# Kernel tuning notes

Hardware: AMD Instinct MI355X
Metric: run time of the kernel (lower is better)

Reference implementation:

```python
import jax, jax.numpy as jnp
import numpy as np

N_EMBD = 512
HEAD_SIZE = 64
B, T = 256, 256


def setup_inputs() -> dict:
    key = jax.random.key(0)
    ks = jax.random.split(key, 7)
    s = 1.0 / np.sqrt(N_EMBD)
    return {
        "x": jax.random.normal(ks[0], (B, T, N_EMBD), dtype=jnp.float32),
        "Wk": jax.random.uniform(ks[1], (N_EMBD, HEAD_SIZE), jnp.float32, -s, s),
        "bk": jax.random.uniform(ks[2], (HEAD_SIZE,), jnp.float32, -s, s),
        "Wq": jax.random.uniform(ks[3], (N_EMBD, HEAD_SIZE), jnp.float32, -s, s),
        "bq": jax.random.uniform(ks[4], (HEAD_SIZE,), jnp.float32, -s, s),
        "Wv": jax.random.uniform(ks[5], (N_EMBD, HEAD_SIZE), jnp.float32, -s, s),
        "bv": jax.random.uniform(ks[6], (HEAD_SIZE,), jnp.float32, -s, s),
    }


def reference(x, Wk, bk, Wq, bq, Wv, bv):
    # Single-head causal self-attention (dropout = identity in eval mode).
    Bq, Tq, C = x.shape
    k = x @ Wk + bk        # [B, T, H]
    q = x @ Wq + bq        # [B, T, H]
    v = x @ Wv + bv        # [B, T, H]
    scale = 1.0 / jnp.sqrt(jnp.asarray(k.shape[-1], x.dtype))
    scores = jnp.einsum('bth,bsh->bts', q, k) * scale  # [B, T, T]
    causal = jnp.tril(jnp.ones((Tq, Tq), dtype=bool))
    scores = jnp.where(causal, scores, -jnp.inf)
    attn = jax.nn.softmax(scores, axis=-1)
    return jnp.einsum('bts,bsh->bth', attn, v)  # [B, T, H]
```

## Files before the change

### kernel.cpp

```cpp
#include <hip/hip_runtime.h>
#include <stdint.h>

typedef __attribute__((ext_vector_type(8))) short bf16x8;
typedef __attribute__((ext_vector_type(4))) float f32x4;

#if __has_builtin(__builtin_amdgcn_exp2f)
#define EXP2F(x) __builtin_amdgcn_exp2f(x)
#else
#define EXP2F(x) exp2f(x)
#endif

__device__ __forceinline__ short f2bf(float f) {
    union { float f; uint32_t u; } c; c.f = f;
    return (short)((c.u + 0x7fffu + ((c.u >> 16) & 1u)) >> 16);
}

__global__ void prep_kernel(const float* __restrict__ Wk, const float* __restrict__ bk,
                            const float* __restrict__ Wq, const float* __restrict__ bq,
                            const float* __restrict__ Wv, const float* __restrict__ bv,
                            short* __restrict__ Wt, float* __restrict__ bcat) {
    const int col = blockIdx.x;
    const float* W; const float* bb; int c0;
    if (col < 64)       { W = Wk; bb = bk; c0 = col; }
    else if (col < 128) { W = Wq; bb = bq; c0 = col - 64; }
    else                { W = Wv; bb = bv; c0 = col - 128; }
    for (int c = threadIdx.x; c < 512; c += blockDim.x)
        Wt[col * 512 + c] = f2bf(W[(size_t)c * 64 + c0]);
    if (threadIdx.x == 0) bcat[col] = bb[c0];
}

__global__ __launch_bounds__(256, 2) void qkv_kernel(
    const float* __restrict__ x, const short* __restrict__ Wt,
    const float* __restrict__ bcat,
    short* __restrict__ Kb, short* __restrict__ Qb, short* __restrict__ Vb) {
    const int tid = threadIdx.x;
    const int wave = tid >> 6, lane = tid & 63;
    const int quad = lane >> 4, l16 = lane & 15;
    const int row0 = blockIdx.x * 128 + wave * 32;

    f32x4 acc[2][12];
#pragma unroll
    for (int m = 0; m < 2; m++)
#pragma unroll
        for (int i = 0; i < 12; i++) acc[m][i] = (f32x4){0.f, 0.f, 0.f, 0.f};

    const float* xr0 = x + (size_t)(row0 + l16) * 512 + quad * 8;
    const float* xr1 = xr0 + (size_t)16 * 512;

    float4 p00 = ((const float4*)xr0)[0];
    float4 p01 = ((const float4*)xr0)[1];
    float4 p10 = ((const float4*)xr1)[0];
    float4 p11 = ((const float4*)xr1)[1];

    for (int c = 0; c < 16; c++) {
        bf16x8 a0, a1;
        a0[0]=f2bf(p00.x); a0[1]=f2bf(p00.y); a0[2]=f2bf(p00.z); a0[3]=f2bf(p00.w);
        a0[4]=f2bf(p01.x); a0[5]=f2bf(p01.y); a0[6]=f2bf(p01.z); a0[7]=f2bf(p01.w);
        a1[0]=f2bf(p10.x); a1[1]=f2bf(p10.y); a1[2]=f2bf(p10.z); a1[3]=f2bf(p10.w);
        a1[4]=f2bf(p11.x); a1[5]=f2bf(p11.y); a1[6]=f2bf(p11.z); a1[7]=f2bf(p11.w);
        if (c < 15) {
            const float* n0 = xr0 + (c + 1) * 32;
            const float* n1 = xr1 + (c + 1) * 32;
            p00 = ((const float4*)n0)[0];
            p01 = ((const float4*)n0)[1];
            p10 = ((const float4*)n1)[0];
            p11 = ((const float4*)n1)[1];
        }
#pragma unroll
        for (int nt = 0; nt < 12; nt++) {
            bf16x8 bfrag = *(const bf16x8*)&Wt[(nt*16 + l16)*512 + c*32 + quad*8];
            acc[0][nt] = __builtin_amdgcn_mfma_f32_16x16x32_bf16(a0, bfrag, acc[0][nt], 0, 0, 0);
            acc[1][nt] = __builtin_amdgcn_mfma_f32_16x16x32_bf16(a1, bfrag, acc[1][nt], 0, 0, 0);
        }
    }

#pragma unroll
    for (int m = 0; m < 2; m++) {
        const int rowbase = row0 + m*16 + quad*4;
#pragma unroll
        for (int nt = 0; nt < 12; nt++) {
            const int col = nt*16 + l16;
            const float bias = bcat[col];
            short* dst = (nt < 4) ? Kb : (nt < 8) ? Qb : Vb;
            const int h = col & 63;
#pragma unroll
            for (int r = 0; r < 4; r++)
                dst[(size_t)(rowbase + r)*64 + h] = f2bf(acc[m][nt][r] + bias);
        }
    }
}

#define KSTR 72
#define VSTR 72
#define PSTR 40

__global__ __launch_bounds__(256, 2) void attn_kernel(
    const short* __restrict__ Kb, const short* __restrict__ Qb,
    const short* __restrict__ Vb, float* __restrict__ out) {
    __shared__ __align__(16) short Ks[256 * KSTR];
    __shared__ __align__(16) short Vt[2][64 * VSTR];
    __shared__ __align__(16) short Ps[4][16 * PSTR];

    const int j = blockIdx.x;
    const int b = blockIdx.y;
    const int tid = threadIdx.x;
    const int wave = tid >> 6, lane = tid & 63;
    const int quad = lane >> 4, l16 = lane & 15;
    const int ntiles = 4 * (j + 1);
    const int nchunks = j + 1;
    const size_t bbase = (size_t)b * (256 * 64);

    const int qrow = j*64 + wave*16 + l16;
    const bf16x8 qf0 = *(const bf16x8*)&Qb[bbase + (size_t)qrow*64 + quad*8];
    const bf16x8 qf1 = *(const bf16x8*)&Qb[bbase + (size_t)qrow*64 + 32 + quad*8];

    {
        const int r = tid >> 2, seg = tid & 3;
        for (int rb = 0; rb < nchunks; rb++) {
            const int row = rb*64 + r;
            const uint4* src = (const uint4*)&Kb[bbase + (size_t)row*64 + seg*16];
            uint4 a0 = src[0], a1 = src[1];
            *(uint4*)&Ks[row*KSTR + seg*16]     = a0;
            *(uint4*)&Ks[row*KSTR + seg*16 + 8] = a1;
        }
    }
    const int vs0 = (tid >> 3) * 2;
    const int vh  = tid & 7;
    uint32_t vregs[8];
    const uint16_t* Vbu = (const uint16_t*)Vb;
#pragma unroll
    for (int i = 0; i < 8; i++) {
        uint32_t lo = Vbu[bbase + (size_t)vs0*64 + vh + 8*i];
        uint32_t hi = Vbu[bbase + (size_t)(vs0 + 1)*64 + vh + 8*i];
        vregs[i] = lo | (hi << 16);
    }
#pragma unroll
    for (int i = 0; i < 8; i++)
        *(uint32_t*)&Vt[0][(vh + 8*i)*VSTR + vs0] = vregs[i];
    __syncthreads();

    f32x4 St[16];
#pragma unroll
    for (int i = 0; i < 16; i++) St[i] = (f32x4){0.f, 0.f, 0.f, 0.f};
#pragma unroll
    for (int nt = 0; nt < 16; nt++) if (nt < ntiles) {
        bf16x8 kf0 = *(const bf16x8*)&Ks[(nt*16 + l16)*KSTR + quad*8];
        bf16x8 kf1 = *(const bf16x8*)&Ks[(nt*16 + l16)*KSTR + 32 + quad*8];
        St[nt] = __builtin_amdgcn_mfma_f32_16x16x32_bf16(qf0, kf0, St[nt], 0, 0, 0);
        St[nt] = __builtin_amdgcn_mfma_f32_16x16x32_bf16(qf1, kf1, St[nt], 0, 0, 0);
    }

    const float sc2 = 0.125f * 1.44269504088896340736f;
    const int rowg0 = j*64 + wave*16 + quad*4;
    float mx[4], ls[4];
#pragma unroll
    for (int r = 0; r < 4; r++) mx[r] = -3.0e38f;
#pragma unroll
    for (int nt = 0; nt < 16; nt++) if (nt < ntiles) {
        const int cs = nt*16 + l16;
#pragma unroll
        for (int r = 0; r < 4; r++) {
            float s = (cs <= rowg0 + r) ? St[nt][r] * sc2 : -3.0e38f;
            St[nt][r] = s;
            mx[r] = fmaxf(mx[r], s);
        }
    }
#pragma unroll
    for (int d = 1; d < 16; d <<= 1)
#pragma unroll
        for (int r = 0; r < 4; r++)
            mx[r] = fmaxf(mx[r], __shfl_xor(mx[r], d, 64));
#pragma unroll
    for (int r = 0; r < 4; r++) ls[r] = 0.f;
#pragma unroll
    for (int nt = 0; nt < 16; nt++) if (nt < ntiles) {
#pragma unroll
        for (int r = 0; r < 4; r++) {
            float p = EXP2F(St[nt][r] - mx[r]);
            St[nt][r] = p;
            ls[r] += p;
        }
    }
#pragma unroll
    for (int d = 1; d < 16; d <<= 1)
#pragma unroll
        for (int r = 0; r < 4; r++)
            ls[r] += __shfl_xor(ls[r], d, 64);

    f32x4 O[4];
#pragma unroll
    for (int i = 0; i < 4; i++) O[i] = (f32x4){0.f, 0.f, 0.f, 0.f};
    short* myP = Ps[wave];

#pragma unroll
    for (int c = 0; c < 4; c++) if (c < nchunks) {
        const int buf = c & 1;
        if (c + 1 < nchunks) {
#pragma unroll
            for (int i = 0; i < 8; i++) {
                uint32_t lo = Vbu[bbase + (size_t)((c+1)*64 + vs0)*64 + vh + 8*i];
                uint32_t hi = Vbu[bbase + (size_t)((c+1)*64 + vs0 + 1)*64 + vh + 8*i];
                vregs[i] = lo | (hi << 16);
            }
        }
#pragma unroll
        for (int sub = 0; sub < 2; sub++) {
#pragma unroll
            for (int t2 = 0; t2 < 2; t2++) {
                const int nt = c*4 + sub*2 + t2;
#pragma unroll
                for (int r = 0; r < 4; r++)
                    myP[(quad*4 + r)*PSTR + t2*16 + l16] = f2bf(St[nt][r]);
            }
            bf16x8 pf = *(const bf16x8*)&myP[l16*PSTR + quad*8];
#pragma unroll
            for (int ht = 0; ht < 4; ht++) {
                bf16x8 vf = *(const bf16x8*)&Vt[buf][(ht*16 + l16)*VSTR + sub*32 + quad*8];
                O[ht] = __builtin_amdgcn_mfma_f32_16x16x32_bf16(pf, vf, O[ht], 0, 0, 0);
            }
        }
        if (c + 1 < nchunks) {
#pragma unroll
            for (int i = 0; i < 8; i++)
                *(uint32_t*)&Vt[(c+1) & 1][(vh + 8*i)*VSTR + vs0] = vregs[i];
        }
        __syncthreads();
    }

    float rls[4];
#pragma unroll
    for (int r = 0; r < 4; r++) rls[r] = 1.0f / ls[r];
    const int orow0 = j*64 + wave*16 + quad*4;
#pragma unroll
    for (int ht = 0; ht < 4; ht++)
#pragma unroll
        for (int r = 0; r < 4; r++)
            out[((size_t)b*256 + orow0 + r)*64 + ht*16 + l16] = O[ht][r] * rls[r];
}

extern "C" void kernel_launch(void* const* d_in, const int* in_sizes, int n_in,
                              void* d_out, int out_size, void* d_ws, size_t ws_size,
                              hipStream_t stream) {
    const float* x  = (const float*)d_in[0];
    const float* Wk = (const float*)d_in[1];
    const float* bk = (const float*)d_in[2];
    const float* Wq = (const float*)d_in[3];
    const float* bq = (const float*)d_in[4];
    const float* Wv = (const float*)d_in[5];
    const float* bv = (const float*)d_in[6];
    float* out = (float*)d_out;

    char* ws = (char*)d_ws;
    short* Wt   = (short*)(ws);
    float* bcat = (float*)(ws + 196608);
    short* Kb   = (short*)(ws + 262144);
    short* Qb   = (short*)(ws + 262144 + 8388608);
    short* Vb   = (short*)(ws + 262144 + 16777216);

    prep_kernel<<<192, 256, 0, stream>>>(Wk, bk, Wq, bq, Wv, bv, Wt, bcat);
    qkv_kernel<<<512, 256, 0, stream>>>(x, Wt, bcat, Kb, Qb, Vb);
    attn_kernel<<<dim3(4, 256), 256, 0, stream>>>(Kb, Qb, Vb, out);
}
```

Baseline: 268.2 us.

## Stage QKV and attention operands via async global-to-LDS copies with swizzled layouts

The QKV projection now double-buffers x and weight tiles into shared memory with async global_load_lds copies and XOR swizzles, after the prep kernel rewrites the weights chunk-major. Outputs are staged in LDS so K and Q are written with wide coalesced stores, and V is written pre-transposed. The attention kernel loads K and the transposed V with async LDS copies into swizzled unpadded buffers, and launches the heaviest causal blocks first. This targets global load latency, uncoalesced 2-byte V gathers and bank conflicts, at the cost of more LDS per block (which may lower occupancy) and extra barriers.

```diff
diff --git a/kernel.cpp b/kernel.cpp
--- a/kernel.cpp
+++ b/kernel.cpp
@@ -15,28 +15,40 @@
     return (short)((c.u + 0x7fffu + ((c.u >> 16) & 1u)) >> 16);
 }
 
+typedef __attribute__((address_space(1))) void gvoid;
+typedef __attribute__((address_space(3))) void lvoid;
+__device__ __forceinline__ void async_cp16(const void* g, void* l) {
+    __builtin_amdgcn_global_load_lds((gvoid*)g, (lvoid*)l, 16, 0, 0);
+}
+
 __global__ void prep_kernel(const float* __restrict__ Wk, const float* __restrict__ bk,
                             const float* __restrict__ Wq, const float* __restrict__ bq,
                             const float* __restrict__ Wv, const float* __restrict__ bv,
-                            short* __restrict__ Wt, float* __restrict__ bcat) {
+                            short* __restrict__ Wt2g, float* __restrict__ bcat) {
     const int col = blockIdx.x;
     const float* W; const float* bb; int c0;
     if (col < 64)       { W = Wk; bb = bk; c0 = col; }
     else if (col < 128) { W = Wq; bb = bq; c0 = col - 64; }
     else                { W = Wv; bb = bv; c0 = col - 128; }
     for (int c = threadIdx.x; c < 512; c += blockDim.x)
-        Wt[col * 512 + c] = f2bf(W[(size_t)c * 64 + c0]);
+        Wt2g[(c >> 5) * (192 * 32) + col * 32 + (c & 31)] = f2bf(W[(size_t)c * 64 + c0]);
     if (threadIdx.x == 0) bcat[col] = bb[c0];
 }
 
 __global__ __launch_bounds__(256, 2) void qkv_kernel(
-    const float* __restrict__ x, const short* __restrict__ Wt,
+    const float* __restrict__ x, const short* __restrict__ Wt2g,
     const float* __restrict__ bcat,
-    short* __restrict__ Kb, short* __restrict__ Qb, short* __restrict__ Vb) {
+    short* __restrict__ Kb, short* __restrict__ Qb, short* __restrict__ Vt) {
+    __shared__ __align__(16) char smem[57344];
+#define XS(bufp)  ((float*)(smem + (bufp) * 16384))
+#define WSB(bufp) ((short*)(smem + 32768 + (bufp) * 12288))
+    short* ce = (short*)smem;
+    const int CEP = 216;
+
     const int tid = threadIdx.x;
     const int wave = tid >> 6, lane = tid & 63;
     const int quad = lane >> 4, l16 = lane & 15;
-    const int row0 = blockIdx.x * 128 + wave * 32;
+    const int row0 = blockIdx.x * 128;
 
     f32x4 acc[2][12];
 #pragma unroll
@@ -44,64 +56,114 @@
 #pragma unroll
         for (int i = 0; i < 12; i++) acc[m][i] = (f32x4){0.f, 0.f, 0.f, 0.f};
 
-    const float* xr0 = x + (size_t)(row0 + l16) * 512 + quad * 8;
-    const float* xr1 = xr0 + (size_t)16 * 512;
-
-    float4 p00 = ((const float4*)xr0)[0];
-    float4 p01 = ((const float4*)xr0)[1];
-    float4 p10 = ((const float4*)xr1)[0];
-    float4 p11 = ((const float4*)xr1)[1];
-
+    const int xr = (lane >> 3);
+    const int xsl = lane & 7;
+    const int wc = lane >> 2;
+    const int wsl = lane & 3;
+
+#define STAGE_X(cc, bufp)                                                          \
+    for (int q = 0; q < 4; q++) {                                                  \
+        const int i = wave * 4 + q;                                                \
+        const int r = i * 8 + xr;                                                  \
+        const int s = xsl ^ ((r & 3) << 1);                                        \
+        async_cp16(x + (size_t)(row0 + r) * 512 + (cc) * 32 + s * 4,               \
+                   smem + (bufp) * 16384 + i * 1024);                              \
+    }
+#define STAGE_W(cc, bufp)                                                          \
+    for (int q = 0; q < 3; q++) {                                                  \
+        const int i = wave * 3 + q;                                                \
+        const int col = i * 16 + wc;                                               \
+        const int s = wsl ^ (col & 3);                                             \
+        async_cp16(Wt2g + ((size_t)(cc) * 192 + col) * 32 + s * 8,                 \
+                   smem + 32768 + (bufp) * 12288 + i * 1024);                      \
+    }
+
+    STAGE_X(0, 0)
+    STAGE_W(0, 0)
+    __syncthreads();
+
+    const int axoff = (quad ^ (l16 & 3)) * 8;
     for (int c = 0; c < 16; c++) {
+        const int buf = c & 1;
+        if (c < 15) { STAGE_X(c + 1, buf ^ 1) STAGE_W(c + 1, buf ^ 1) }
+        const float* pa0 = XS(buf) + (wave * 32 + l16) * 32 + axoff;
+        const float* pa1 = XS(buf) + (wave * 32 + 16 + l16) * 32 + axoff;
+        f32x4 u0 = *(const f32x4*)pa0, u1 = *(const f32x4*)(pa0 + 4);
+        f32x4 u2 = *(const f32x4*)pa1, u3 = *(const f32x4*)(pa1 + 4);
         bf16x8 a0, a1;
-        a0[0]=f2bf(p00.x); a0[1]=f2bf(p00.y); a0[2]=f2bf(p00.z); a0[3]=f2bf(p00.w);
-        a0[4]=f2bf(p01.x); a0[5]=f2bf(p01.y); a0[6]=f2bf(p01.z); a0[7]=f2bf(p01.w);
-        a1[0]=f2bf(p10.x); a1[1]=f2bf(p10.y); a1[2]=f2bf(p10.z); a1[3]=f2bf(p10.w);
-        a1[4]=f2bf(p11.x); a1[5]=f2bf(p11.y); a1[6]=f2bf(p11.z); a1[7]=f2bf(p11.w);
-        if (c < 15) {
-            const float* n0 = xr0 + (c + 1) * 32;
-            const float* n1 = xr1 + (c + 1) * 32;
-            p00 = ((const float4*)n0)[0];
-            p01 = ((const float4*)n0)[1];
-            p10 = ((const float4*)n1)[0];
-            p11 = ((const float4*)n1)[1];
-        }
+#pragma unroll
+        for (int i = 0; i < 4; i++) { a0[i] = f2bf(u0[i]); a0[4+i] = f2bf(u1[i]); }
+#pragma unroll
+        for (int i = 0; i < 4; i++) { a1[i] = f2bf(u2[i]); a1[4+i] = f2bf(u3[i]); }
+        const short* wb = WSB(buf);
 #pragma unroll
         for (int nt = 0; nt < 12; nt++) {
-            bf16x8 bfrag = *(const bf16x8*)&Wt[(nt*16 + l16)*512 + c*32 + quad*8];
+            bf16x8 bfrag = *(const bf16x8*)&wb[(nt * 16 + l16) * 32 + axoff];
             acc[0][nt] = __builtin_amdgcn_mfma_f32_16x16x32_bf16(a0, bfrag, acc[0][nt], 0, 0, 0);
             acc[1][nt] = __builtin_amdgcn_mfma_f32_16x16x32_bf16(a1, bfrag, acc[1][nt], 0, 0, 0);
         }
+        __syncthreads();
     }
 
 #pragma unroll
     for (int m = 0; m < 2; m++) {
-        const int rowbase = row0 + m*16 + quad*4;
+        const int lrow = wave * 32 + m * 16 + quad * 4;
 #pragma unroll
         for (int nt = 0; nt < 12; nt++) {
-            const int col = nt*16 + l16;
+            const int col = nt * 16 + l16;
             const float bias = bcat[col];
-            short* dst = (nt < 4) ? Kb : (nt < 8) ? Qb : Vb;
-            const int h = col & 63;
 #pragma unroll
             for (int r = 0; r < 4; r++)
-                dst[(size_t)(rowbase + r)*64 + h] = f2bf(acc[m][nt][r] + bias);
-        }
-    }
-}
-
-#define KSTR 72
-#define VSTR 72
+                ce[(lrow + r) * CEP + col] = f2bf(acc[m][nt][r] + bias);
+        }
+    }
+    __syncthreads();
+
+    {
+        const int row = tid >> 1, half = tid & 1;
+        const size_t gro = (size_t)(row0 + row) * 64 + half * 32;
+#pragma unroll
+        for (int j4 = 0; j4 < 4; j4++) {
+            uint4 kv = *(const uint4*)&ce[row * CEP + half * 32 + j4 * 8];
+            *(uint4*)&Kb[gro + j4 * 8] = kv;
+            uint4 qv = *(const uint4*)&ce[row * CEP + 64 + half * 32 + j4 * 8];
+            *(uint4*)&Qb[gro + j4 * 8] = qv;
+        }
+    }
+    {
+        const int h = tid >> 2, sq = tid & 3;
+        const size_t vbase = (size_t)(row0 >> 8) * 16384 + (size_t)h * 256 + (row0 & 255) + sq * 32;
+        const uint16_t* ceu = (const uint16_t*)ce;
+#pragma unroll
+        for (int g = 0; g < 4; g++) {
+            uint4 v;
+            uint32_t* vw = (uint32_t*)&v;
+#pragma unroll
+            for (int p = 0; p < 4; p++) {
+                const int sl = sq * 32 + g * 8 + p * 2;
+                uint32_t lo = ceu[sl * CEP + 128 + h];
+                uint32_t hi = ceu[(sl + 1) * CEP + 128 + h];
+                vw[p] = lo | (hi << 16);
+            }
+            *(uint4*)&Vt[vbase + g * 8] = v;
+        }
+    }
+#undef XS
+#undef WSB
+#undef STAGE_X
+#undef STAGE_W
+}
+
 #define PSTR 40
 
 __global__ __launch_bounds__(256, 2) void attn_kernel(
     const short* __restrict__ Kb, const short* __restrict__ Qb,
-    const short* __restrict__ Vb, float* __restrict__ out) {
-    __shared__ __align__(16) short Ks[256 * KSTR];
-    __shared__ __align__(16) short Vt[2][64 * VSTR];
+    const short* __restrict__ Vt, float* __restrict__ out) {
+    __shared__ __align__(16) short Ks[256 * 64];
+    __shared__ __align__(16) short Vts[2][64 * 64];
     __shared__ __align__(16) short Ps[4][16 * PSTR];
 
-    const int j = blockIdx.x;
+    const int j = 3 - blockIdx.x;
     const int b = blockIdx.y;
     const int tid = threadIdx.x;
     const int wave = tid >> 6, lane = tid & 63;
@@ -110,33 +172,27 @@
     const int nchunks = j + 1;
     const size_t bbase = (size_t)b * (256 * 64);
 
-    const int qrow = j*64 + wave*16 + l16;
-    const bf16x8 qf0 = *(const bf16x8*)&Qb[bbase + (size_t)qrow*64 + quad*8];
-    const bf16x8 qf1 = *(const bf16x8*)&Qb[bbase + (size_t)qrow*64 + 32 + quad*8];
-
-    {
-        const int r = tid >> 2, seg = tid & 3;
-        for (int rb = 0; rb < nchunks; rb++) {
-            const int row = rb*64 + r;
-            const uint4* src = (const uint4*)&Kb[bbase + (size_t)row*64 + seg*16];
-            uint4 a0 = src[0], a1 = src[1];
-            *(uint4*)&Ks[row*KSTR + seg*16]     = a0;
-            *(uint4*)&Ks[row*KSTR + seg*16 + 8] = a1;
-        }
-    }
-    const int vs0 = (tid >> 3) * 2;
-    const int vh  = tid & 7;
-    uint32_t vregs[8];
-    const uint16_t* Vbu = (const uint16_t*)Vb;
-#pragma unroll
-    for (int i = 0; i < 8; i++) {
-        uint32_t lo = Vbu[bbase + (size_t)vs0*64 + vh + 8*i];
-        uint32_t hi = Vbu[bbase + (size_t)(vs0 + 1)*64 + vh + 8*i];
-        vregs[i] = lo | (hi << 16);
-    }
-#pragma unroll
-    for (int i = 0; i < 8; i++)
-        *(uint32_t*)&Vt[0][(vh + 8*i)*VSTR + vs0] = vregs[i];
+    const int sr = lane >> 3;
+    const int ssl = lane & 7;
+    const int ssrc = (ssl ^ sr) * 8;
+
+    for (int q = 0; q < 2 * nchunks; q++) {
+        const int i = q * 4 + wave;
+        const int row = i * 8 + sr;
+        async_cp16(Kb + bbase + (size_t)row * 64 + ssrc, (char*)Ks + i * 1024);
+    }
+#define STAGE_V(cc, bufp)                                                          \
+    for (int q = 0; q < 2; q++) {                                                  \
+        const int i = q * 4 + wave;                                                \
+        const int h = i * 8 + sr;                                                  \
+        async_cp16(Vt + (size_t)b * 16384 + (size_t)h * 256 + (cc) * 64 + ssrc,    \
+                   (char*)Vts[bufp] + i * 1024);                                   \
+    }
+    STAGE_V(0, 0)
+
+    const int qrow = j * 64 + wave * 16 + l16;
+    const bf16x8 qf0 = *(const bf16x8*)&Qb[bbase + (size_t)qrow * 64 + quad * 8];
+    const bf16x8 qf1 = *(const bf16x8*)&Qb[bbase + (size_t)qrow * 64 + 32 + quad * 8];
     __syncthreads();
 
     f32x4 St[16];
@@ -144,20 +200,21 @@
     for (int i = 0; i < 16; i++) St[i] = (f32x4){0.f, 0.f, 0.f, 0.f};
 #pragma unroll
     for (int nt = 0; nt < 16; nt++) if (nt < ntiles) {
-        bf16x8 kf0 = *(const bf16x8*)&Ks[(nt*16 + l16)*KSTR + quad*8];
-        bf16x8 kf1 = *(const bf16x8*)&Ks[(nt*16 + l16)*KSTR + 32 + quad*8];
+        const short* kr = &Ks[(nt * 16 + l16) * 64];
+        bf16x8 kf0 = *(const bf16x8*)&kr[(quad ^ (l16 & 7)) * 8];
+        bf16x8 kf1 = *(const bf16x8*)&kr[((quad + 4) ^ (l16 & 7)) * 8];
         St[nt] = __builtin_amdgcn_mfma_f32_16x16x32_bf16(qf0, kf0, St[nt], 0, 0, 0);
         St[nt] = __builtin_amdgcn_mfma_f32_16x16x32_bf16(qf1, kf1, St[nt], 0, 0, 0);
     }
 
     const float sc2 = 0.125f * 1.44269504088896340736f;
-    const int rowg0 = j*64 + wave*16 + quad*4;
+    const int rowg0 = j * 64 + wave * 16 + quad * 4;
     float mx[4], ls[4];
 #pragma unroll
     for (int r = 0; r < 4; r++) mx[r] = -3.0e38f;
 #pragma unroll
     for (int nt = 0; nt < 16; nt++) if (nt < ntiles) {
-        const int cs = nt*16 + l16;
+        const int cs = nt * 16 + l16;
 #pragma unroll
         for (int r = 0; r < 4; r++) {
             float s = (cs <= rowg0 + r) ? St[nt][r] * sc2 : -3.0e38f;
@@ -195,47 +252,36 @@
 #pragma unroll
     for (int c = 0; c < 4; c++) if (c < nchunks) {
         const int buf = c & 1;
-        if (c + 1 < nchunks) {
-#pragma unroll
-            for (int i = 0; i < 8; i++) {
-                uint32_t lo = Vbu[bbase + (size_t)((c+1)*64 + vs0)*64 + vh + 8*i];
-                uint32_t hi = Vbu[bbase + (size_t)((c+1)*64 + vs0 + 1)*64 + vh + 8*i];
-                vregs[i] = lo | (hi << 16);
+        if (c + 1 < nchunks) { STAGE_V(c + 1, buf ^ 1) }
+#pragma unroll
+        for (int sub = 0; sub < 2; sub++) {
+#pragma unroll
+            for (int t2 = 0; t2 < 2; t2++) {
+                const int nt = c * 4 + sub * 2 + t2;
+#pragma unroll
+                for (int r = 0; r < 4; r++)
+                    myP[(quad * 4 + r) * PSTR + t2 * 16 + l16] = f2bf(St[nt][r]);
             }
-        }
-#pragma unroll
-        for (int sub = 0; sub < 2; sub++) {
-#pragma unroll
-            for (int t2 = 0; t2 < 2; t2++) {
-                const int nt = c*4 + sub*2 + t2;
-#pragma unroll
-                for (int r = 0; r < 4; r++)
-                    myP[(quad*4 + r)*PSTR + t2*16 + l16] = f2bf(St[nt][r]);
-            }
-            bf16x8 pf = *(const bf16x8*)&myP[l16*PSTR + quad*8];
+            bf16x8 pf = *(const bf16x8*)&myP[l16 * PSTR + quad * 8];
 #pragma unroll
             for (int ht = 0; ht < 4; ht++) {
-                bf16x8 vf = *(const bf16x8*)&Vt[buf][(ht*16 + l16)*VSTR + sub*32 + quad*8];
+                bf16x8 vf = *(const bf16x8*)&Vts[buf][(ht * 16 + l16) * 64 +
+                                                      (((sub * 4 + quad) ^ (l16 & 7)) * 8)];
                 O[ht] = __builtin_amdgcn_mfma_f32_16x16x32_bf16(pf, vf, O[ht], 0, 0, 0);
             }
         }
-        if (c + 1 < nchunks) {
-#pragma unroll
-            for (int i = 0; i < 8; i++)
-                *(uint32_t*)&Vt[(c+1) & 1][(vh + 8*i)*VSTR + vs0] = vregs[i];
-        }
         __syncthreads();
     }
 
     float rls[4];
 #pragma unroll
     for (int r = 0; r < 4; r++) rls[r] = 1.0f / ls[r];
-    const int orow0 = j*64 + wave*16 + quad*4;
+    const int orow0 = j * 64 + wave * 16 + quad * 4;
 #pragma unroll
     for (int ht = 0; ht < 4; ht++)
 #pragma unroll
         for (int r = 0; r < 4; r++)
-            out[((size_t)b*256 + orow0 + r)*64 + ht*16 + l16] = O[ht][r] * rls[r];
+            out[((size_t)b * 256 + orow0 + r) * 64 + ht * 16 + l16] = O[ht][r] * rls[r];
 }
 
 extern "C" void kernel_launch(void* const* d_in, const int* in_sizes, int n_in,
@@ -251,13 +297,13 @@
     float* out = (float*)d_out;
 
     char* ws = (char*)d_ws;
-    short* Wt   = (short*)(ws);
+    short* Wt2g = (short*)(ws);
     float* bcat = (float*)(ws + 196608);
     short* Kb   = (short*)(ws + 262144);
     short* Qb   = (short*)(ws + 262144 + 8388608);
-    short* Vb   = (short*)(ws + 262144 + 16777216);
-
-    prep_kernel<<<192, 256, 0, stream>>>(Wk, bk, Wq, bq, Wv, bv, Wt, bcat);
-    qkv_kernel<<<512, 256, 0, stream>>>(x, Wt, bcat, Kb, Qb, Vb);
-    attn_kernel<<<dim3(4, 256), 256, 0, stream>>>(Kb, Qb, Vb, out);
-}
+    short* Vt   = (short*)(ws + 262144 + 16777216);
+
+    prep_kernel<<<192, 256, 0, stream>>>(Wk, bk, Wq, bq, Wv, bv, Wt2g, bcat);
+    qkv_kernel<<<512, 256, 0, stream>>>(x, Wt2g, bcat, Kb, Qb, Vt);
+    attn_kernel<<<dim3(4, 256), 256, 0, stream>>>(Kb, Qb, Vt, out);
+}
```

Measured after the change: 233.2 us. -13.0%, faster.

## Fuse QKV projection and causal attention into one kernel per batch

Applied to the files above, without the earlier changes.

Merges the QKV projection and attention kernels into a single kernel with one 512-thread block per batch element. K, Q and transposed V are kept in XOR-swizzled shared memory, so the bf16 K/Q/V round trip through global memory is gone. Each wave takes a pair of query tiles (t and 15-t) to even out the causal work, and the weight layout is regrouped by k-chunk for more contiguous loads. In exchange, only 256 blocks of about 106 KB shared memory each are launched, which lowers parallelism and occupancy.

```diff
diff --git a/kernel.cpp b/kernel.cpp
--- a/kernel.cpp
+++ b/kernel.cpp
@@ -18,25 +18,33 @@
 __global__ void prep_kernel(const float* __restrict__ Wk, const float* __restrict__ bk,
                             const float* __restrict__ Wq, const float* __restrict__ bq,
                             const float* __restrict__ Wv, const float* __restrict__ bv,
-                            short* __restrict__ Wt, float* __restrict__ bcat) {
+                            short* __restrict__ Wt2g, float* __restrict__ bcat) {
     const int col = blockIdx.x;
     const float* W; const float* bb; int c0;
     if (col < 64)       { W = Wk; bb = bk; c0 = col; }
     else if (col < 128) { W = Wq; bb = bq; c0 = col - 64; }
     else                { W = Wv; bb = bv; c0 = col - 128; }
     for (int c = threadIdx.x; c < 512; c += blockDim.x)
-        Wt[col * 512 + c] = f2bf(W[(size_t)c * 64 + c0]);
+        Wt2g[(c >> 5) * (192 * 32) + col * 32 + (c & 31)] = f2bf(W[(size_t)c * 64 + c0]);
     if (threadIdx.x == 0) bcat[col] = bb[c0];
 }
 
-__global__ __launch_bounds__(256, 2) void qkv_kernel(
-    const float* __restrict__ x, const short* __restrict__ Wt,
-    const float* __restrict__ bcat,
-    short* __restrict__ Kb, short* __restrict__ Qb, short* __restrict__ Vb) {
+#define PSTR 40
+
+__global__ __launch_bounds__(512, 2) void fused_kernel(
+    const float* __restrict__ x, const short* __restrict__ Wt2g,
+    const float* __restrict__ bcat, float* __restrict__ out) {
+    extern __shared__ __align__(16) char smem[];
+    short* Ks  = (short*)smem;
+    short* Qs  = (short*)(smem + 32768);
+    short* Vts = (short*)(smem + 65536);
+    short* Ps  = (short*)(smem + 98304);
+
     const int tid = threadIdx.x;
     const int wave = tid >> 6, lane = tid & 63;
     const int quad = lane >> 4, l16 = lane & 15;
-    const int row0 = blockIdx.x * 128 + wave * 32;
+    const int b = blockIdx.x;
+    const int ta = wave, tb = 15 - wave;
 
     f32x4 acc[2][12];
 #pragma unroll
@@ -44,31 +52,28 @@
 #pragma unroll
         for (int i = 0; i < 12; i++) acc[m][i] = (f32x4){0.f, 0.f, 0.f, 0.f};
 
-    const float* xr0 = x + (size_t)(row0 + l16) * 512 + quad * 8;
-    const float* xr1 = xr0 + (size_t)16 * 512;
-
-    float4 p00 = ((const float4*)xr0)[0];
-    float4 p01 = ((const float4*)xr0)[1];
-    float4 p10 = ((const float4*)xr1)[0];
-    float4 p11 = ((const float4*)xr1)[1];
-
-    for (int c = 0; c < 16; c++) {
+    const float* xA0 = x + ((size_t)b * 256 + ta * 16 + l16) * 512 + quad * 8;
+    const float* xA1 = x + ((size_t)b * 256 + tb * 16 + l16) * 512 + quad * 8;
+
+    f32x4 p00 = *(const f32x4*)xA0, p01 = *(const f32x4*)(xA0 + 4);
+    f32x4 p10 = *(const f32x4*)xA1, p11 = *(const f32x4*)(xA1 + 4);
+
+    for (int kc = 0; kc < 16; kc++) {
         bf16x8 a0, a1;
-        a0[0]=f2bf(p00.x); a0[1]=f2bf(p00.y); a0[2]=f2bf(p00.z); a0[3]=f2bf(p00.w);
-        a0[4]=f2bf(p01.x); a0[5]=f2bf(p01.y); a0[6]=f2bf(p01.z); a0[7]=f2bf(p01.w);
-        a1[0]=f2bf(p10.x); a1[1]=f2bf(p10.y); a1[2]=f2bf(p10.z); a1[3]=f2bf(p10.w);
-        a1[4]=f2bf(p11.x); a1[5]=f2bf(p11.y); a1[6]=f2bf(p11.z); a1[7]=f2bf(p11.w);
-        if (c < 15) {
-            const float* n0 = xr0 + (c + 1) * 32;
-            const float* n1 = xr1 + (c + 1) * 32;
-            p00 = ((const float4*)n0)[0];
-            p01 = ((const float4*)n0)[1];
-            p10 = ((const float4*)n1)[0];
-            p11 = ((const float4*)n1)[1];
-        }
+#pragma unroll
+        for (int i = 0; i < 4; i++) { a0[i] = f2bf(p00[i]); a0[4 + i] = f2bf(p01[i]); }
+#pragma unroll
+        for (int i = 0; i < 4; i++) { a1[i] = f2bf(p10[i]); a1[4 + i] = f2bf(p11[i]); }
+        if (kc < 15) {
+            p00 = *(const f32x4*)(xA0 + (kc + 1) * 32);
+            p01 = *(const f32x4*)(xA0 + (kc + 1) * 32 + 4);
+            p10 = *(const f32x4*)(xA1 + (kc + 1) * 32);
+            p11 = *(const f32x4*)(xA1 + (kc + 1) * 32 + 4);
+        }
+        const short* wkc = Wt2g + kc * 6144 + l16 * 32 + quad * 8;
 #pragma unroll
         for (int nt = 0; nt < 12; nt++) {
-            bf16x8 bfrag = *(const bf16x8*)&Wt[(nt*16 + l16)*512 + c*32 + quad*8];
+            bf16x8 bfrag = *(const bf16x8*)(wkc + nt * 512);
             acc[0][nt] = __builtin_amdgcn_mfma_f32_16x16x32_bf16(a0, bfrag, acc[0][nt], 0, 0, 0);
             acc[1][nt] = __builtin_amdgcn_mfma_f32_16x16x32_bf16(a1, bfrag, acc[1][nt], 0, 0, 0);
         }
@@ -76,166 +81,117 @@
 
 #pragma unroll
     for (int m = 0; m < 2; m++) {
-        const int rowbase = row0 + m*16 + quad*4;
+        const int t = m ? tb : ta;
 #pragma unroll
         for (int nt = 0; nt < 12; nt++) {
-            const int col = nt*16 + l16;
+            const int col = nt * 16 + l16;
             const float bias = bcat[col];
-            short* dst = (nt < 4) ? Kb : (nt < 8) ? Qb : Vb;
             const int h = col & 63;
 #pragma unroll
+            for (int r = 0; r < 4; r++) {
+                const short v = f2bf(acc[m][nt][r] + bias);
+                const int row = t * 16 + quad * 4 + r;
+                if (nt < 4)
+                    Ks[row * 64 + (((h >> 3) ^ (row & 7)) << 3) + (h & 7)] = v;
+                else if (nt < 8)
+                    Qs[row * 64 + (((h >> 3) ^ (row & 7)) << 3) + (h & 7)] = v;
+                else
+                    Vts[h * 256 + (((row >> 3) ^ (h & 7)) << 3) + (row & 7)] = v;
+            }
+        }
+    }
+    __syncthreads();
+
+    const float sc2 = 0.125f * 1.44269504088896340736f;
+    short* myP = Ps + wave * (16 * PSTR);
+
+#pragma unroll
+    for (int ti = 0; ti < 2; ti++) {
+        const int t = ti ? tb : ta;
+        const int qrow = t * 16 + l16;
+        const int sw = l16 & 7;
+        bf16x8 qf0 = *(const bf16x8*)&Qs[qrow * 64 + ((quad ^ sw) << 3)];
+        bf16x8 qf1 = *(const bf16x8*)&Qs[qrow * 64 + (((4 + quad) ^ sw) << 3)];
+
+        f32x4 St[16];
+#pragma unroll
+        for (int i = 0; i < 16; i++) St[i] = (f32x4){0.f, 0.f, 0.f, 0.f};
+#pragma unroll
+        for (int nt = 0; nt < 16; nt++) if (nt <= t) {
+            const int krow = nt * 16 + l16;
+            bf16x8 kf0 = *(const bf16x8*)&Ks[krow * 64 + ((quad ^ sw) << 3)];
+            bf16x8 kf1 = *(const bf16x8*)&Ks[krow * 64 + (((4 + quad) ^ sw) << 3)];
+            St[nt] = __builtin_amdgcn_mfma_f32_16x16x32_bf16(qf0, kf0, St[nt], 0, 0, 0);
+            St[nt] = __builtin_amdgcn_mfma_f32_16x16x32_bf16(qf1, kf1, St[nt], 0, 0, 0);
+        }
+
+        const int rowq = t * 16 + quad * 4;
+        float mx[4], ls[4];
+#pragma unroll
+        for (int r = 0; r < 4; r++) mx[r] = -3.0e38f;
+#pragma unroll
+        for (int nt = 0; nt < 16; nt++) if (nt <= t) {
+            const int cs = nt * 16 + l16;
+#pragma unroll
+            for (int r = 0; r < 4; r++) {
+                float s = (cs <= rowq + r) ? St[nt][r] * sc2 : -3.0e38f;
+                St[nt][r] = s;
+                mx[r] = fmaxf(mx[r], s);
+            }
+        }
+#pragma unroll
+        for (int d = 1; d < 16; d <<= 1)
+#pragma unroll
             for (int r = 0; r < 4; r++)
-                dst[(size_t)(rowbase + r)*64 + h] = f2bf(acc[m][nt][r] + bias);
-        }
+                mx[r] = fmaxf(mx[r], __shfl_xor(mx[r], d, 64));
+#pragma unroll
+        for (int r = 0; r < 4; r++) ls[r] = 0.f;
+#pragma unroll
+        for (int nt = 0; nt < 16; nt++) if (nt <= t) {
+#pragma unroll
+            for (int r = 0; r < 4; r++) {
+                float p = EXP2F(St[nt][r] - mx[r]);
+                St[nt][r] = p;
+                ls[r] += p;
+            }
+        }
+#pragma unroll
+        for (int d = 1; d < 16; d <<= 1)
+#pragma unroll
+            for (int r = 0; r < 4; r++)
+                ls[r] += __shfl_xor(ls[r], d, 64);
+
+        f32x4 O[4];
+#pragma unroll
+        for (int i = 0; i < 4; i++) O[i] = (f32x4){0.f, 0.f, 0.f, 0.f};
+        const int nch = (t + 2) >> 1;
+#pragma unroll
+        for (int c2 = 0; c2 < 8; c2++) if (c2 < nch) {
+#pragma unroll
+            for (int t2i = 0; t2i < 2; t2i++) {
+                const int nt = c2 * 2 + t2i;
+#pragma unroll
+                for (int r = 0; r < 4; r++)
+                    myP[(quad * 4 + r) * PSTR + t2i * 16 + l16] = f2bf(St[nt][r]);
+            }
+            bf16x8 pf = *(const bf16x8*)&myP[l16 * PSTR + quad * 8];
+#pragma unroll
+            for (int ht = 0; ht < 4; ht++) {
+                const int h = ht * 16 + l16;
+                bf16x8 vf = *(const bf16x8*)&Vts[h * 256 + ((((c2 * 4 + quad)) ^ (h & 7)) << 3)];
+                O[ht] = __builtin_amdgcn_mfma_f32_16x16x32_bf16(pf, vf, O[ht], 0, 0, 0);
+            }
+        }
+
+        float rls[4];
+#pragma unroll
+        for (int r = 0; r < 4; r++) rls[r] = 1.0f / ls[r];
+#pragma unroll
+        for (int ht = 0; ht < 4; ht++)
+#pragma unroll
+            for (int r = 0; r < 4; r++)
+                out[((size_t)b * 256 + rowq + r) * 64 + ht * 16 + l16] = O[ht][r] * rls[r];
     }
-}
-
-#define KSTR 72
-#define VSTR 72
-#define PSTR 40
-
-__global__ __launch_bounds__(256, 2) void attn_kernel(
-    const short* __restrict__ Kb, const short* __restrict__ Qb,
-    const short* __restrict__ Vb, float* __restrict__ out) {
-    __shared__ __align__(16) short Ks[256 * KSTR];
-    __shared__ __align__(16) short Vt[2][64 * VSTR];
-    __shared__ __align__(16) short Ps[4][16 * PSTR];
-
-    const int j = blockIdx.x;
-    const int b = blockIdx.y;
-    const int tid = threadIdx.x;
-    const int wave = tid >> 6, lane = tid & 63;
-    const int quad = lane >> 4, l16 = lane & 15;
-    const int ntiles = 4 * (j + 1);
-    const int nchunks = j + 1;
-    const size_t bbase = (size_t)b * (256 * 64);
-
-    const int qrow = j*64 + wave*16 + l16;
-    const bf16x8 qf0 = *(const bf16x8*)&Qb[bbase + (size_t)qrow*64 + quad*8];
-    const bf16x8 qf1 = *(const bf16x8*)&Qb[bbase + (size_t)qrow*64 + 32 + quad*8];
-
-    {
-        const int r = tid >> 2, seg = tid & 3;
-        for (int rb = 0; rb < nchunks; rb++) {
-            const int row = rb*64 + r;
-            const uint4* src = (const uint4*)&Kb[bbase + (size_t)row*64 + seg*16];
-            uint4 a0 = src[0], a1 = src[1];
-            *(uint4*)&Ks[row*KSTR + seg*16]     = a0;
-            *(uint4*)&Ks[row*KSTR + seg*16 + 8] = a1;
-        }
-    }
-    const int vs0 = (tid >> 3) * 2;
-    const int vh  = tid & 7;
-    uint32_t vregs[8];
-    const uint16_t* Vbu = (const uint16_t*)Vb;
-#pragma unroll
-    for (int i = 0; i < 8; i++) {
-        uint32_t lo = Vbu[bbase + (size_t)vs0*64 + vh + 8*i];
-        uint32_t hi = Vbu[bbase + (size_t)(vs0 + 1)*64 + vh + 8*i];
-        vregs[i] = lo | (hi << 16);
-    }
-#pragma unroll
-    for (int i = 0; i < 8; i++)
-        *(uint32_t*)&Vt[0][(vh + 8*i)*VSTR + vs0] = vregs[i];
-    __syncthreads();
-
-    f32x4 St[16];
-#pragma unroll
-    for (int i = 0; i < 16; i++) St[i] = (f32x4){0.f, 0.f, 0.f, 0.f};
-#pragma unroll
-    for (int nt = 0; nt < 16; nt++) if (nt < ntiles) {
-        bf16x8 kf0 = *(const bf16x8*)&Ks[(nt*16 + l16)*KSTR + quad*8];
-        bf16x8 kf1 = *(const bf16x8*)&Ks[(nt*16 + l16)*KSTR + 32 + quad*8];
-        St[nt] = __builtin_amdgcn_mfma_f32_16x16x32_bf16(qf0, kf0, St[nt], 0, 0, 0);
-        St[nt] = __builtin_amdgcn_mfma_f32_16x16x32_bf16(qf1, kf1, St[nt], 0, 0, 0);
-    }
-
-    const float sc2 = 0.125f * 1.44269504088896340736f;
-    const int rowg0 = j*64 + wave*16 + quad*4;
-    float mx[4], ls[4];
-#pragma unroll
-    for (int r = 0; r < 4; r++) mx[r] = -3.0e38f;
-#pragma unroll
-    for (int nt = 0; nt < 16; nt++) if (nt < ntiles) {
-        const int cs = nt*16 + l16;
-#pragma unroll
-        for (int r = 0; r < 4; r++) {
-            float s = (cs <= rowg0 + r) ? St[nt][r] * sc2 : -3.0e38f;
-            St[nt][r] = s;
-            mx[r] = fmaxf(mx[r], s);
-        }
-    }
-#pragma unroll
-    for (int d = 1; d < 16; d <<= 1)
-#pragma unroll
-        for (int r = 0; r < 4; r++)
-            mx[r] = fmaxf(mx[r], __shfl_xor(mx[r], d, 64));
-#pragma unroll
-    for (int r = 0; r < 4; r++) ls[r] = 0.f;
-#pragma unroll
-    for (int nt = 0; nt < 16; nt++) if (nt < ntiles) {
-#pragma unroll
-        for (int r = 0; r < 4; r++) {
-            float p = EXP2F(St[nt][r] - mx[r]);
-            St[nt][r] = p;
-            ls[r] += p;
-        }
-    }
-#pragma unroll
-    for (int d = 1; d < 16; d <<= 1)
-#pragma unroll
-        for (int r = 0; r < 4; r++)
-            ls[r] += __shfl_xor(ls[r], d, 64);
-
-    f32x4 O[4];
-#pragma unroll
-    for (int i = 0; i < 4; i++) O[i] = (f32x4){0.f, 0.f, 0.f, 0.f};
-    short* myP = Ps[wave];
-
-#pragma unroll
-    for (int c = 0; c < 4; c++) if (c < nchunks) {
-        const int buf = c & 1;
-        if (c + 1 < nchunks) {
-#pragma unroll
-            for (int i = 0; i < 8; i++) {
-                uint32_t lo = Vbu[bbase + (size_t)((c+1)*64 + vs0)*64 + vh + 8*i];
-                uint32_t hi = Vbu[bbase + (size_t)((c+1)*64 + vs0 + 1)*64 + vh + 8*i];
-                vregs[i] = lo | (hi << 16);
-            }
-        }
-#pragma unroll
-        for (int sub = 0; sub < 2; sub++) {
-#pragma unroll
-            for (int t2 = 0; t2 < 2; t2++) {
-                const int nt = c*4 + sub*2 + t2;
-#pragma unroll
-                for (int r = 0; r < 4; r++)
-                    myP[(quad*4 + r)*PSTR + t2*16 + l16] = f2bf(St[nt][r]);
-            }
-            bf16x8 pf = *(const bf16x8*)&myP[l16*PSTR + quad*8];
-#pragma unroll
-            for (int ht = 0; ht < 4; ht++) {
-                bf16x8 vf = *(const bf16x8*)&Vt[buf][(ht*16 + l16)*VSTR + sub*32 + quad*8];
-                O[ht] = __builtin_amdgcn_mfma_f32_16x16x32_bf16(pf, vf, O[ht], 0, 0, 0);
-            }
-        }
-        if (c + 1 < nchunks) {
-#pragma unroll
-            for (int i = 0; i < 8; i++)
-                *(uint32_t*)&Vt[(c+1) & 1][(vh + 8*i)*VSTR + vs0] = vregs[i];
-        }
-        __syncthreads();
-    }
-
-    float rls[4];
-#pragma unroll
-    for (int r = 0; r < 4; r++) rls[r] = 1.0f / ls[r];
-    const int orow0 = j*64 + wave*16 + quad*4;
-#pragma unroll
-    for (int ht = 0; ht < 4; ht++)
-#pragma unroll
-        for (int r = 0; r < 4; r++)
-            out[((size_t)b*256 + orow0 + r)*64 + ht*16 + l16] = O[ht][r] * rls[r];
 }
 
 extern "C" void kernel_launch(void* const* d_in, const int* in_sizes, int n_in,
@@ -251,13 +207,13 @@
     float* out = (float*)d_out;
 
     char* ws = (char*)d_ws;
-    short* Wt   = (short*)(ws);
+    short* Wt2g = (short*)(ws);
     float* bcat = (float*)(ws + 196608);
-    short* Kb   = (short*)(ws + 262144);
-    short* Qb   = (short*)(ws + 262144 + 8388608);
-    short* Vb   = (short*)(ws + 262144 + 16777216);
-
-    prep_kernel<<<192, 256, 0, stream>>>(Wk, bk, Wq, bq, Wv, bv, Wt, bcat);
-    qkv_kernel<<<512, 256, 0, stream>>>(x, Wt, bcat, Kb, Qb, Vb);
-    attn_kernel<<<dim3(4, 256), 256, 0, stream>>>(Kb, Qb, Vb, out);
-}
+
+    const int smem_bytes = 108544;
+    (void)hipFuncSetAttribute((const void*)fused_kernel,
+                              hipFuncAttributeMaxDynamicSharedMemorySize, smem_bytes);
+
+    prep_kernel<<<192, 256, 0, stream>>>(Wk, bk, Wq, bq, Wv, bv, Wt2g, bcat);
+    fused_kernel<<<256, 512, smem_bytes, stream>>>(x, Wt2g, bcat, out);
+}
```

After: 229.6 us. 1.17x faster.
